# Optimization experiments

Hardware: AMD Instinct MI355X
Metric: run time of the kernel (lower is better)

## Reference

```python
import jax, jax.numpy as jnp
import numpy as np

D_MODEL = 1024
N_TILES = 16
BATCH = 32768
THRESH = 0.3


def setup_inputs() -> dict:
    key = jax.random.key(0)
    k_x, k_sig, k_w, k_b = jax.random.split(key, 4)
    x = jax.random.normal(k_x, (BATCH, D_MODEL), dtype=jnp.float32)
    # nn.Parameter(torch.randn(n_tiles, d_model) * 0.5)
    signatures_raw = jax.random.normal(k_sig, (N_TILES, D_MODEL), dtype=jnp.float32) * 0.5
    # nn.Linear(d_model, d_model) default init: U(-1/sqrt(fan_in), 1/sqrt(fan_in))
    bound = 1.0 / np.sqrt(D_MODEL)
    W = jax.random.uniform(k_w, (N_TILES, D_MODEL, D_MODEL), dtype=jnp.float32, minval=-bound, maxval=bound)
    b = jax.random.uniform(k_b, (N_TILES, D_MODEL), dtype=jnp.float32, minval=-bound, maxval=bound)
    return {"x": x, "signatures_raw": signatures_raw, "W": W, "b": b}


def _quantize_ternary(s):
    # straight-through ternary: forward value is q, gradient is identity
    q = jnp.where(s > THRESH, 1.0, jnp.where(s < -THRESH, -1.0, 0.0))
    return s + jax.lax.stop_gradient(q - s)


def reference(x, signatures_raw, W, b):
    sigs = _quantize_ternary(signatures_raw)          # [E, D]
    scores = x @ sigs.T                               # [B, E]
    tile_indices = jnp.argmax(scores, axis=-1)        # [B]
    out = jnp.zeros_like(x)
    # fixed small loop over experts: masked combine of per-expert Linear+ReLU
    for e in range(N_TILES):
        y = jax.nn.relu(x @ W[e].T + b[e])            # [B, D]
        out = out + jnp.where((tile_indices == e)[:, None], y, 0.0)
    out = out + x                                     # residual
    return out, tile_indices
```

## Files before the change

kernel.cpp:

```cpp
#include <hip/hip_runtime.h>
#include <hip/hip_bf16.h>

#define BATCH   32768
#define DM      1024
#define NE      16
#define THRESHF 0.3f
#define MARGIN  0.02f

#define CTRL_OFF 131072
#define QBF_OFF  139264
#define PERM_OFF 172032
#define XBF_OFF  319488
#define WB_OFF   67428352ull
#define WS_NEED  (WB_OFF + (size_t)NE * DM * DM * 2)

typedef __attribute__((ext_vector_type(8))) short bf16x8;
typedef __attribute__((ext_vector_type(4))) float f32x4;

#define MFMA16(a, b, c) __builtin_amdgcn_mfma_f32_16x16x32_bf16(a, b, c, 0, 0, 0)

static __device__ __forceinline__ unsigned short f2bf(float f) {
    union { float f; unsigned u; } v; v.f = f;
    unsigned r = (v.u + 0x7FFFu + ((v.u >> 16) & 1u)) >> 16;
    return (unsigned short)r;
}
static __device__ __forceinline__ float bf2f(unsigned short h) {
    union { unsigned u; float f; } v; v.u = ((unsigned)h) << 16;
    return v.f;
}

static __device__ __forceinline__ void gload_lds16(const void* g, void* s) {
    __builtin_amdgcn_global_load_lds(
        (const __attribute__((address_space(1))) void*)g,
        (__attribute__((address_space(3))) void*)s, 16, 0, 0);
}

static __device__ __forceinline__ int tile_base(const unsigned* ctrl, int* tb) {
    int acc = 0;
#pragma unroll
    for (int e = 0; e < NE; ++e) {
        tb[e] = acc;
        acc += (int)((ctrl[e * 16] + 127u) >> 7);
    }
    tb[NE] = acc;
    return acc;
}

__global__ void k_init(const float* __restrict__ sig, unsigned* __restrict__ ctrl,
                       int* __restrict__ perm, unsigned short* __restrict__ Qbf) {
    const int t = blockIdx.x * 256 + threadIdx.x;
    if (t < 544) ctrl[t] = 0;
    if (t < 1024) {
        unsigned pm = 0, mm = 0;
#pragma unroll
        for (int e = 0; e < NE; ++e) {
            float s = sig[e * DM + t];
            pm |= (s > THRESHF ? 1u : 0u) << e;
            mm |= (s < -THRESHF ? 1u : 0u) << e;
        }
        ctrl[1024 + t] = pm | (mm << 16);
    }
    if (t < 9216) ((int4*)perm)[t] = make_int4(0, 0, 0, 0);
    {
        float s = sig[t];
        Qbf[t] = s > THRESHF ? (unsigned short)0x3F80u
                             : (s < -THRESHF ? (unsigned short)0xBF80u : (unsigned short)0u);
    }
}

__global__ __launch_bounds__(256) void k_router(const float* __restrict__ x,
                                                const unsigned short* __restrict__ Qbf,
                                                unsigned* __restrict__ ctrl,
                                                int* __restrict__ idx,
                                                float* __restrict__ outIdx,
                                                unsigned short* __restrict__ Xbf,
                                                int writeXbf) {
    __shared__ float S[4][64][4];
    const int t = threadIdx.x, w = t >> 6, l = t & 63;
    const int lc = l & 15, lr = l >> 4;
    const int row0 = blockIdx.x * 16;
    const unsigned* packT = ctrl + 1024;

    const float* ax = x + (size_t)(row0 + lc) * DM + lr * 8;
    const unsigned short* qx = Qbf + (size_t)lc * DM + lr * 8;
    unsigned short* xb = Xbf + (size_t)(row0 + lc) * DM + lr * 8;

    f32x4 acc = (f32x4){0.f, 0.f, 0.f, 0.f};

    for (int kt = w * 4; kt < w * 4 + 4; ++kt) {
#pragma unroll
        for (int h = 0; h < 2; ++h) {
            const int ko = kt * 64 + h * 32;
            float4 v0 = *(const float4*)(ax + ko);
            float4 v1 = *(const float4*)(ax + ko + 4);
            bf16x8 q = *(const bf16x8*)(qx + ko);

            float f[8] = {v0.x, v0.y, v0.z, v0.w, v1.x, v1.y, v1.z, v1.w};
            bf16x8 ah, al;
#pragma unroll
            for (int j = 0; j < 8; ++j) {
                unsigned short hi = f2bf(f[j]);
                float r = f[j] - bf2f(hi);
                ah[j] = (short)hi;
                al[j] = (short)f2bf(r);
            }
            if (writeXbf) *(bf16x8*)(xb + ko) = ah;
            acc = MFMA16(ah, q, acc);
            acc = MFMA16(al, q, acc);
        }
    }

    *(f32x4*)&S[w][l][0] = acc;
    __syncthreads();
    if (w != 0) return;

#pragma unroll
    for (int s = 1; s < 4; ++s) acc += *(const f32x4*)&S[s][l][0];

    float bv[4]; int bi[4]; float gap[4];
#pragma unroll
    for (int reg = 0; reg < 4; ++reg) {
        float v = acc[reg]; int i = lc; float s = -3.4e38f;
#pragma unroll
        for (int m = 1; m < 16; m <<= 1) {
            float ov = __shfl_xor(v, m, 64);
            int oi = __shfl_xor(i, m, 64);
            float os = __shfl_xor(s, m, 64);
            bool take = (ov > v) || (ov == v && oi < i);
            float loser = take ? v : ov;
            v = take ? ov : v;
            i = take ? oi : i;
            s = fmaxf(fmaxf(s, os), loser);
        }
        bv[reg] = v; bi[reg] = i; gap[reg] = v - s;
    }

    unsigned flagsw = 0;
#pragma unroll
    for (int reg = 0; reg < 4; ++reg)
        flagsw |= (gap[reg] < MARGIN ? 1u : 0u) << reg;

    if (__any(lc == 0 && flagsw != 0)) {
#pragma unroll
        for (int reg = 0; reg < 4; ++reg) {
            for (int g = 0; g < 4; ++g) {
                const unsigned fw = __shfl(flagsw, g * 16, 64);
                if ((fw >> reg) & 1u) {
                    const int row = row0 + g * 4 + reg;
                    const float* xr = x + (size_t)row * DM;
                    float xv[16]; unsigned mk[16];
#pragma unroll
                    for (int k2 = 0; k2 < 16; ++k2) {
                        xv[k2] = xr[k2 * 64 + l];
                        mk[k2] = packT[k2 * 64 + l];
                    }
                    double best = 0.0; int bbi = 0;
                    for (int e = 0; e < 16; ++e) {
                        double a = 0.0;
#pragma unroll
                        for (int k2 = 0; k2 < 16; ++k2) {
                            const int pb = (int)((mk[k2] >> e) & 1u);
                            const int mb = (int)((mk[k2] >> (16 + e)) & 1u);
                            a += pb ? (double)xv[k2] : (mb ? -(double)xv[k2] : 0.0);
                        }
#pragma unroll
                        for (int m = 1; m < 64; m <<= 1) a += __shfl_xor(a, m, 64);
                        if (e == 0 || a > best) { best = a; bbi = e; }
                    }
                    if (lr == g && lc == 0) bi[reg] = bbi;
                }
            }
        }
    }

    if (lc == 0) {
#pragma unroll
        for (int reg = 0; reg < 4; ++reg) {
            const int row = row0 + lr * 4 + reg;
            idx[row] = bi[reg];
            outIdx[row] = (float)bi[reg];
            atomicAdd(&ctrl[bi[reg] * 16], 1u);
        }
    }
}

__global__ __launch_bounds__(256) void k_permconv(const int* __restrict__ idx,
                                                  unsigned* __restrict__ ctrl,
                                                  int* __restrict__ perm,
                                                  const float* __restrict__ W,
                                                  unsigned short* __restrict__ Wb) {
    if (blockIdx.x >= 128) {
        const size_t g = ((size_t)(blockIdx.x - 128) * 256 + threadIdx.x) * 8;
        float4 a = *(const float4*)&W[g];
        float4 b = *(const float4*)&W[g + 4];
        *(ushort4*)&Wb[g]     = make_ushort4(f2bf(a.x), f2bf(a.y), f2bf(a.z), f2bf(a.w));
        *(ushort4*)&Wb[g + 4] = make_ushort4(f2bf(b.x), f2bf(b.y), f2bf(b.z), f2bf(b.w));
        return;
    }
    __shared__ unsigned hcnt[16];
    __shared__ unsigned hbase[16];
    const int t = threadIdx.x;
    const int row = blockIdx.x * 256 + t;
    int tb[NE + 1];
    tile_base(ctrl, tb);
    if (t < 16) hcnt[t] = 0;
    __syncthreads();
    const int e = idx[row];
    const unsigned lrank = atomicAdd(&hcnt[e], 1u);
    __syncthreads();
    if (t < 16) hbase[t] = atomicAdd(&ctrl[256 + t * 16], hcnt[t]);
    __syncthreads();
    perm[tb[e] * 128 + hbase[e] + lrank] = row;
}

__global__ __launch_bounds__(512) void k_gemm(
        const unsigned short* __restrict__ Xbf,
        const unsigned short* __restrict__ Wb,
        const float* __restrict__ bias,
        const int* __restrict__ perm,
        const unsigned* __restrict__ ctrl,
        float* __restrict__ out) {
    __shared__ unsigned short A_lds[3][128 * 32];
    __shared__ unsigned short B_lds[3][256 * 32];

    int tb[NE + 1];
    const int total = tile_base(ctrl, tb);

    int bx, ny;
    {
        const int flat = blockIdx.x;
        const int xcd = flat & 7, s2 = flat >> 3;
        bx = xcd * 34 + (s2 >> 2);
        ny = s2 & 3;
    }
    if (bx >= total) return;
    int e = 0;
    while (e < NE - 1 && tb[e + 1] <= bx) ++e;
    const int valid = (int)ctrl[e * 16] - (bx - tb[e]) * 128;
    const int n0 = ny * 256;

    const int t = threadIdx.x, w = t >> 6, l = t & 63;
    const int wr = w >> 2, wc = w & 3;
    const int lc = l & 15, lr = l >> 4;
    const int hsw = ((t & 3) - ((t >> 3) & 3)) & 3;
    const int ssw = (lr + (lc >> 1)) & 3;

    f32x4 acc[4][4];
#pragma unroll
    for (int m = 0; m < 4; ++m)
#pragma unroll
        for (int n = 0; n < 4; ++n) acc[m][n] = (f32x4){0.f, 0.f, 0.f, 0.f};

    const size_t aRowBase = (size_t)bx * 128;
    const unsigned short* Bg = Wb + ((size_t)e * DM + n0) * DM;

    const int prow = perm[aRowBase + (t >> 2)];
    const unsigned short* a0 = Xbf + (size_t)prow * DM + hsw * 8;
    const unsigned short* b0 = Bg + (size_t)(t >> 2) * DM + hsw * 8;
    const unsigned short* b1 = Bg + (size_t)(128 + (t >> 2)) * DM + hsw * 8;

    auto STAGE = [&](int kt, int buf) {
        const int ko = kt * 32;
        gload_lds16(a0 + ko, &A_lds[buf][(size_t)(w * 64) * 8]);
        gload_lds16(b0 + ko, &B_lds[buf][(size_t)(w * 64) * 8]);
        gload_lds16(b1 + ko, &B_lds[buf][(size_t)(512 + w * 64) * 8]);
    };

    STAGE(0, 0);
    STAGE(1, 1);

    const int NT = DM / 32;
    int cur = 0;
    for (int kt = 0; kt < NT; ++kt) {
        if (kt + 1 < NT) asm volatile("s_waitcnt vmcnt(3)" ::: "memory");
        else             asm volatile("s_waitcnt vmcnt(0)" ::: "memory");
        __builtin_amdgcn_sched_barrier(0);
        __builtin_amdgcn_s_barrier();
        __builtin_amdgcn_sched_barrier(0);

        if (kt + 2 < NT) {
            const int nb = (cur + 2 >= 3) ? cur - 1 : cur + 2;
            STAGE(kt + 2, nb);
        }

        bf16x8 af[4], bf[4];
#pragma unroll
        for (int m = 0; m < 4; ++m)
            af[m] = *(const bf16x8*)&A_lds[cur][(wr * 64 + m * 16 + lc) * 32 + ssw * 8];
#pragma unroll
        for (int n = 0; n < 4; ++n)
            bf[n] = *(const bf16x8*)&B_lds[cur][(wc * 64 + n * 16 + lc) * 32 + ssw * 8];
#pragma unroll
        for (int m = 0; m < 4; ++m)
#pragma unroll
            for (int n = 0; n < 4; ++n)
                acc[m][n] = MFMA16(af[m], bf[n], acc[m][n]);

        cur = (cur + 1 >= 3) ? 0 : cur + 1;
    }

    float bvv[4];
#pragma unroll
    for (int n = 0; n < 4; ++n) bvv[n] = bias[e * DM + n0 + wc * 64 + n * 16 + lc];

#pragma unroll
    for (int m = 0; m < 4; ++m) {
#pragma unroll
        for (int reg = 0; reg < 4; ++reg) {
            const int rit = wr * 64 + m * 16 + lr * 4 + reg;
            if (rit < valid) {
                const int orow = perm[aRowBase + rit];
                float* op = out + (size_t)orow * DM;
                const unsigned short* xr = Xbf + (size_t)orow * DM;
#pragma unroll
                for (int n = 0; n < 4; ++n) {
                    const int col = n0 + wc * 64 + n * 16 + lc;
                    float v = acc[m][n][reg] + bvv[n];
                    v = v > 0.f ? v : 0.f;
                    op[col] = v + bf2f(xr[col]);
                }
            }
        }
    }
}

__global__ __launch_bounds__(256) void k_gemm_small(
        const float* __restrict__ x, const float* __restrict__ W,
        const float* __restrict__ bias, const int* __restrict__ perm,
        const unsigned* __restrict__ ctrl, float* __restrict__ out) {
    __shared__ unsigned short A_lds[128 * 32];
    __shared__ unsigned short B_lds[128 * 32];
    int tb[NE + 1];
    const int total = tile_base(ctrl, tb);
    int bx, ny;
    {
        const int flat = blockIdx.x;
        const int xcd = flat & 7, s2 = flat >> 3;
        bx = xcd * 34 + (s2 >> 3);
        ny = s2 & 7;
    }
    if (bx >= total) return;
    int e = 0;
    while (e < NE - 1 && tb[e + 1] <= bx) ++e;
    const int valid = (int)ctrl[e * 16] - (bx - tb[e]) * 128;
    const int n0 = ny * 128;
    const int t = threadIdx.x, w = t >> 6, l = t & 63;
    const int wr = w >> 1, wc = w & 1;
    const int lc = l & 15, lr = l >> 4;
    const int hsw = ((t & 3) - ((t >> 3) & 3)) & 3;
    const int ssw = (lr + (lc >> 1)) & 3;

    f32x4 acc[4][4];
#pragma unroll
    for (int m = 0; m < 4; ++m)
#pragma unroll
        for (int n = 0; n < 4; ++n) acc[m][n] = (f32x4){0.f, 0.f, 0.f, 0.f};
    const size_t aRowBase = (size_t)bx * 128;

    for (int kt = 0; kt < DM / 32; ++kt) {
        __syncthreads();
#pragma unroll
        for (int rd = 0; rd < 2; ++rd) {
            const int c = rd * 256 + t;
            const int r = c >> 2;
            const float* wp = W + ((size_t)e * DM + n0 + r) * DM + kt * 32 + hsw * 8;
            float4 q0 = *(const float4*)wp;
            float4 q1 = *(const float4*)(wp + 4);
            *(ushort4*)&B_lds[c * 8]     = make_ushort4(f2bf(q0.x), f2bf(q0.y), f2bf(q0.z), f2bf(q0.w));
            *(ushort4*)&B_lds[c * 8 + 4] = make_ushort4(f2bf(q1.x), f2bf(q1.y), f2bf(q1.z), f2bf(q1.w));
            ushort4 p0 = make_ushort4(0, 0, 0, 0), p1 = p0;
            if (r < valid) {
                const int orow = perm[aRowBase + r];
                const float* xp = x + (size_t)orow * DM + kt * 32 + hsw * 8;
                float4 u0 = *(const float4*)xp;
                float4 u1 = *(const float4*)(xp + 4);
                p0 = make_ushort4(f2bf(u0.x), f2bf(u0.y), f2bf(u0.z), f2bf(u0.w));
                p1 = make_ushort4(f2bf(u1.x), f2bf(u1.y), f2bf(u1.z), f2bf(u1.w));
            }
            *(ushort4*)&A_lds[c * 8]     = p0;
            *(ushort4*)&A_lds[c * 8 + 4] = p1;
        }
        __syncthreads();
        bf16x8 af[4], bf[4];
#pragma unroll
        for (int m = 0; m < 4; ++m)
            af[m] = *(const bf16x8*)&A_lds[(wr * 64 + m * 16 + lc) * 32 + ssw * 8];
#pragma unroll
        for (int n = 0; n < 4; ++n)
            bf[n] = *(const bf16x8*)&B_lds[(wc * 64 + n * 16 + lc) * 32 + ssw * 8];
#pragma unroll
        for (int m = 0; m < 4; ++m)
#pragma unroll
            for (int n = 0; n < 4; ++n)
                acc[m][n] = MFMA16(af[m], bf[n], acc[m][n]);
    }

    float bvv[4];
#pragma unroll
    for (int n = 0; n < 4; ++n) bvv[n] = bias[e * DM + n0 + wc * 64 + n * 16 + lc];
#pragma unroll
    for (int m = 0; m < 4; ++m)
#pragma unroll
        for (int reg = 0; reg < 4; ++reg) {
            const int rit = wr * 64 + m * 16 + lr * 4 + reg;
            if (rit < valid) {
                const int orow = perm[aRowBase + rit];
                const float* xr = x + (size_t)orow * DM;
                float* op = out + (size_t)orow * DM;
#pragma unroll
                for (int n = 0; n < 4; ++n) {
                    const int col = n0 + wc * 64 + n * 16 + lc;
                    float v = acc[m][n][reg] + bvv[n];
                    v = v > 0.f ? v : 0.f;
                    op[col] = v + xr[col];
                }
            }
        }
}

extern "C" void kernel_launch(void* const* d_in, const int* in_sizes, int n_in,
                              void* d_out, int out_size, void* d_ws, size_t ws_size,
                              hipStream_t stream) {
    const float* x    = (const float*)d_in[0];
    const float* sig  = (const float*)d_in[1];
    const float* W    = (const float*)d_in[2];
    const float* bias = (const float*)d_in[3];
    float* out = (float*)d_out;
    float* outIdx = out + (size_t)BATCH * DM;

    char* ws = (char*)d_ws;
    int* idx = (int*)ws;
    unsigned* ctrl = (unsigned*)(ws + CTRL_OFF);
    unsigned short* Qbf = (unsigned short*)(ws + QBF_OFF);
    int* perm = (int*)(ws + PERM_OFF);
    unsigned short* Xbf = (unsigned short*)(ws + XBF_OFF);
    unsigned short* Wb = (unsigned short*)(ws + WB_OFF);

    const bool full = ws_size >= WS_NEED;

    k_init<<<64, 256, 0, stream>>>(sig, ctrl, perm, Qbf);
    k_router<<<2048, 256, 0, stream>>>(x, Qbf, ctrl, idx, outIdx, Xbf, full ? 1 : 0);
    k_permconv<<<full ? 8320 : 128, 256, 0, stream>>>(idx, ctrl, perm, W, Wb);
    if (full) {
        k_gemm<<<1088, 512, 0, stream>>>(Xbf, Wb, bias, perm, ctrl, out);
    } else {
        k_gemm_small<<<2176, 256, 0, stream>>>(x, W, bias, perm, ctrl, out);
    }
}
```

Baseline: 222.6 us.

## Enlarge grouped GEMM row tile from 128 to 256 rows per block

Expert row groups are padded to 256 rows instead of 128, and each GEMM block now computes a 256x256 output tile with 8x4 MFMA accumulators per wave. The permutation and tile bases are parametrised on the group size, and the grid shrinks to 576 blocks. The aim is to halve weight-tile reloads per output row and raise arithmetic intensity. In exchange, accumulator register pressure rises, LDS use grows, and more padding is wasted per expert, which may lower occupancy and leave the tail unbalanced.

```diff
diff --git a/kernel.cpp b/kernel.cpp
--- a/kernel.cpp
+++ b/kernel.cpp
@@ -35,12 +35,12 @@
         (__attribute__((address_space(3))) void*)s, 16, 0, 0);
 }
 
-static __device__ __forceinline__ int tile_base(const unsigned* ctrl, int* tb) {
+static __device__ __forceinline__ int tile_base(const unsigned* ctrl, int* tb, int G) {
     int acc = 0;
 #pragma unroll
     for (int e = 0; e < NE; ++e) {
         tb[e] = acc;
-        acc += (int)((ctrl[e * 16] + 127u) >> 7);
+        acc += (int)((ctrl[e * 16] + (unsigned)(G - 1)) / (unsigned)G);
     }
     tb[NE] = acc;
     return acc;
@@ -188,7 +188,8 @@
                                                   unsigned* __restrict__ ctrl,
                                                   int* __restrict__ perm,
                                                   const float* __restrict__ W,
-                                                  unsigned short* __restrict__ Wb) {
+                                                  unsigned short* __restrict__ Wb,
+                                                  int G) {
     if (blockIdx.x >= 128) {
         const size_t g = ((size_t)(blockIdx.x - 128) * 256 + threadIdx.x) * 8;
         float4 a = *(const float4*)&W[g];
@@ -202,7 +203,7 @@
     const int t = threadIdx.x;
     const int row = blockIdx.x * 256 + t;
     int tb[NE + 1];
-    tile_base(ctrl, tb);
+    tile_base(ctrl, tb, G);
     if (t < 16) hcnt[t] = 0;
     __syncthreads();
     const int e = idx[row];
@@ -210,7 +211,7 @@
     __syncthreads();
     if (t < 16) hbase[t] = atomicAdd(&ctrl[256 + t * 16], hcnt[t]);
     __syncthreads();
-    perm[tb[e] * 128 + hbase[e] + lrank] = row;
+    perm[tb[e] * G + hbase[e] + lrank] = row;
 }
 
 __global__ __launch_bounds__(512) void k_gemm(
@@ -220,23 +221,23 @@
         const int* __restrict__ perm,
         const unsigned* __restrict__ ctrl,
         float* __restrict__ out) {
-    __shared__ unsigned short A_lds[3][128 * 32];
+    __shared__ unsigned short A_lds[3][256 * 32];
     __shared__ unsigned short B_lds[3][256 * 32];
 
     int tb[NE + 1];
-    const int total = tile_base(ctrl, tb);
+    const int total = tile_base(ctrl, tb, 256);
 
     int bx, ny;
     {
         const int flat = blockIdx.x;
         const int xcd = flat & 7, s2 = flat >> 3;
-        bx = xcd * 34 + (s2 >> 2);
+        bx = xcd * 18 + (s2 >> 2);
         ny = s2 & 3;
     }
     if (bx >= total) return;
     int e = 0;
     while (e < NE - 1 && tb[e + 1] <= bx) ++e;
-    const int valid = (int)ctrl[e * 16] - (bx - tb[e]) * 128;
+    const int valid = (int)ctrl[e * 16] - (bx - tb[e]) * 256;
     const int n0 = ny * 256;
 
     const int t = threadIdx.x, w = t >> 6, l = t & 63;
@@ -245,23 +246,27 @@
     const int hsw = ((t & 3) - ((t >> 3) & 3)) & 3;
     const int ssw = (lr + (lc >> 1)) & 3;
 
-    f32x4 acc[4][4];
-#pragma unroll
-    for (int m = 0; m < 4; ++m)
+    f32x4 acc[8][4];
+#pragma unroll
+    for (int m = 0; m < 8; ++m)
 #pragma unroll
         for (int n = 0; n < 4; ++n) acc[m][n] = (f32x4){0.f, 0.f, 0.f, 0.f};
 
-    const size_t aRowBase = (size_t)bx * 128;
+    const size_t aRowBase = (size_t)bx * 256;
     const unsigned short* Bg = Wb + ((size_t)e * DM + n0) * DM;
 
-    const int prow = perm[aRowBase + (t >> 2)];
-    const unsigned short* a0 = Xbf + (size_t)prow * DM + hsw * 8;
-    const unsigned short* b0 = Bg + (size_t)(t >> 2) * DM + hsw * 8;
-    const unsigned short* b1 = Bg + (size_t)(128 + (t >> 2)) * DM + hsw * 8;
+    const int r0 = t >> 2;
+    const int prow0 = perm[aRowBase + r0];
+    const int prow1 = perm[aRowBase + 128 + r0];
+    const unsigned short* a0 = Xbf + (size_t)prow0 * DM + hsw * 8;
+    const unsigned short* a1 = Xbf + (size_t)prow1 * DM + hsw * 8;
+    const unsigned short* b0 = Bg + (size_t)r0 * DM + hsw * 8;
+    const unsigned short* b1 = Bg + (size_t)(128 + r0) * DM + hsw * 8;
 
     auto STAGE = [&](int kt, int buf) {
         const int ko = kt * 32;
         gload_lds16(a0 + ko, &A_lds[buf][(size_t)(w * 64) * 8]);
+        gload_lds16(a1 + ko, &A_lds[buf][(size_t)(512 + w * 64) * 8]);
         gload_lds16(b0 + ko, &B_lds[buf][(size_t)(w * 64) * 8]);
         gload_lds16(b1 + ko, &B_lds[buf][(size_t)(512 + w * 64) * 8]);
     };
@@ -272,7 +277,7 @@
     const int NT = DM / 32;
     int cur = 0;
     for (int kt = 0; kt < NT; ++kt) {
-        if (kt + 1 < NT) asm volatile("s_waitcnt vmcnt(3)" ::: "memory");
+        if (kt + 1 < NT) asm volatile("s_waitcnt vmcnt(4)" ::: "memory");
         else             asm volatile("s_waitcnt vmcnt(0)" ::: "memory");
         __builtin_amdgcn_sched_barrier(0);
         __builtin_amdgcn_s_barrier();
@@ -283,18 +288,17 @@
             STAGE(kt + 2, nb);
         }
 
-        bf16x8 af[4], bf[4];
-#pragma unroll
-        for (int m = 0; m < 4; ++m)
-            af[m] = *(const bf16x8*)&A_lds[cur][(wr * 64 + m * 16 + lc) * 32 + ssw * 8];
+        bf16x8 bf[4];
 #pragma unroll
         for (int n = 0; n < 4; ++n)
             bf[n] = *(const bf16x8*)&B_lds[cur][(wc * 64 + n * 16 + lc) * 32 + ssw * 8];
 #pragma unroll
-        for (int m = 0; m < 4; ++m)
+        for (int m = 0; m < 8; ++m) {
+            bf16x8 af = *(const bf16x8*)&A_lds[cur][(wr * 128 + m * 16 + lc) * 32 + ssw * 8];
 #pragma unroll
             for (int n = 0; n < 4; ++n)
-                acc[m][n] = MFMA16(af[m], bf[n], acc[m][n]);
+                acc[m][n] = MFMA16(af, bf[n], acc[m][n]);
+        }
 
         cur = (cur + 1 >= 3) ? 0 : cur + 1;
     }
@@ -304,10 +308,10 @@
     for (int n = 0; n < 4; ++n) bvv[n] = bias[e * DM + n0 + wc * 64 + n * 16 + lc];
 
 #pragma unroll
-    for (int m = 0; m < 4; ++m) {
+    for (int m = 0; m < 8; ++m) {
 #pragma unroll
         for (int reg = 0; reg < 4; ++reg) {
-            const int rit = wr * 64 + m * 16 + lr * 4 + reg;
+            const int rit = wr * 128 + m * 16 + lr * 4 + reg;
             if (rit < valid) {
                 const int orow = perm[aRowBase + rit];
                 float* op = out + (size_t)orow * DM;
@@ -331,7 +335,7 @@
     __shared__ unsigned short A_lds[128 * 32];
     __shared__ unsigned short B_lds[128 * 32];
     int tb[NE + 1];
-    const int total = tile_base(ctrl, tb);
+    const int total = tile_base(ctrl, tb, 128);
     int bx, ny;
     {
         const int flat = blockIdx.x;
@@ -437,12 +441,13 @@
     unsigned short* Wb = (unsigned short*)(ws + WB_OFF);
 
     const bool full = ws_size >= WS_NEED;
+    const int G = full ? 256 : 128;
 
     k_init<<<64, 256, 0, stream>>>(sig, ctrl, perm, Qbf);
     k_router<<<2048, 256, 0, stream>>>(x, Qbf, ctrl, idx, outIdx, Xbf, full ? 1 : 0);
-    k_permconv<<<full ? 8320 : 128, 256, 0, stream>>>(idx, ctrl, perm, W, Wb);
+    k_permconv<<<full ? 8320 : 128, 256, 0, stream>>>(idx, ctrl, perm, W, Wb, G);
     if (full) {
-        k_gemm<<<1088, 512, 0, stream>>>(Xbf, Wb, bias, perm, ctrl, out);
+        k_gemm<<<576, 512, 0, stream>>>(Xbf, Wb, bias, perm, ctrl, out);
     } else {
         k_gemm_small<<<2176, 256, 0, stream>>>(x, W, bias, perm, ctrl, out);
     }
```

Measured after the change: 281.6 us. 1.26x slower.
